# Kernel tuning notes

Measured on AMD Instinct MI355X. Metric: run time of the kernel, lower is better.

The kernel has to match this reference:

```python
import jax, jax.numpy as jnp
import numpy as np

D_K = 128
D_V = 128
SEQ_LEN = 2048


def setup_inputs() -> dict:
    key = jax.random.key(0)
    kq, kk, kv = jax.random.split(key, 3)
    q = jax.random.normal(kq, (SEQ_LEN, D_K), dtype=jnp.float32)
    k = jax.random.normal(kk, (SEQ_LEN, D_K), dtype=jnp.float32)
    v = jax.random.normal(kv, (SEQ_LEN, D_V), dtype=jnp.float32)
    return {"q": q, "k": k, "v": v}


def _step(carry, qkv):
    J, Svv, Sqv, Sqq, l = carry
    q, k, v = qkv
    l = l + 1
    fl = l.astype(J.dtype)
    # update_correlations: running means of outer products
    Svv = (fl - 1.0) / fl * Svv + jnp.outer(v, v) / fl
    Sqv = (fl - 1.0) / fl * Sqv + jnp.outer(q, v) / fl
    Sqq = (fl - 1.0) / fl * Sqq + jnp.outer(q, q) / fl

    first = l == 1

    # ecological params (J: [d_v, d_k], Sqv: [d_k, d_v], Sqq: [d_k, d_k])
    s_J = jnp.einsum('vk,kv->', J, Sqv)            # trace(J @ Sigma_qv)
    s_l = k @ Sqv @ v
    A_JJ = jnp.einsum('vk,kj,vj->', J, Sqq, J)     # trace(J Sqq J^T)
    A_ll = (v @ v) * (k @ Sqq @ k)
    A_Jl = v @ J @ Sqq @ k

    # safe denominators (unused branches must not produce NaN under where)
    A_JJ_s = jnp.where(first | (A_JJ == 0), 1.0, A_JJ)
    A_ll_s = jnp.where(first | (A_ll == 0), 1.0, A_ll)
    denom = A_JJ * A_ll - A_Jl ** 2
    denom_s = jnp.where(first | (denom == 0), 1.0, denom)

    margin = s_l - A_Jl * (s_J / A_JJ_s)

    wf = (A_ll * s_J - A_Jl * s_l) / denom_s
    wi = (A_JJ * s_l - A_Jl * s_J) / denom_s
    # nonnegativity constraints (check omega_i first, as in the source)
    wf_c = jnp.where(wi <= 0, s_J / A_JJ_s, jnp.where(wf <= 0, 0.0, wf))
    wi_c = jnp.where(wi <= 0, 0.0, jnp.where(wf <= 0, s_l / A_ll_s, wi))

    do_update = margin > 0
    vk = jnp.outer(v, k)
    J_upd = jnp.where(do_update, wf_c * J + wi_c * vk, J)
    J_new = jnp.where(first, vk, J_upd)
    updated = first | do_update

    # compute_cost with updated J and correlations
    cost = (0.5 * jnp.trace(Svv)
            - jnp.einsum('vk,kv->', J_new, Sqv)
            + 0.5 * jnp.einsum('vk,kj,vj->', J_new, Sqq, J_new))

    return (J_new, Svv, Sqv, Sqq, l), (cost, updated)


def _run(q, k, v):
    d_k, d_v = q.shape[-1], v.shape[-1]
    init = (jnp.zeros((d_v, d_k), q.dtype),
            jnp.zeros((d_v, d_v), q.dtype),
            jnp.zeros((d_k, d_v), q.dtype),
            jnp.zeros((d_k, d_k), q.dtype),
            jnp.int32(0))
    (J, _, _, _, _), (costs, updated) = jax.lax.scan(_step, init, (q, k, v))
    return costs, updated, J


def reference(q, k, v):
    return _run(q, k, v)
```

## Files before the change

### kernel.cpp

```cpp
#include <hip/hip_runtime.h>

#define SEQ 2048
#define D 128

typedef float v2f __attribute__((ext_vector_type(2)));
typedef float v4f __attribute__((ext_vector_type(4)));
#define LO2(v) __builtin_shufflevector(v, v, 0, 1)
#define HI2(v) __builtin_shufflevector(v, v, 2, 3)

__global__ __launch_bounds__(256) void precompute_kernel(
    const float* __restrict__ q, const float* __restrict__ k, const float* __restrict__ v,
    float* __restrict__ U, float* __restrict__ sl, float* __restrict__ kqq,
    float* __restrict__ vv, float* __restrict__ kq_adj, float* __restrict__ vv_adj,
    float* __restrict__ kU_adj, double* __restrict__ invl)
{
    const int s = blockIdx.x;
    const int tid = threadIdx.x;

    __shared__ float ks[D];
    __shared__ float vs[D];
    __shared__ float alpha[SEQ];
    __shared__ float red[8];
    __shared__ float upart[256];

    if (tid < D) ks[tid] = k[s * D + tid];
    else if (tid < 2 * D) vs[tid - D] = v[s * D + (tid - D)];
    __syncthreads();

    float p_a2 = 0.f, p_ab = 0.f;
    for (int i = tid; i <= s; i += 256) {
        const float4* qr = (const float4*)(q + (size_t)i * D);
        const float4* vr = (const float4*)(v + (size_t)i * D);
        float a = 0.f, b = 0.f;
#pragma unroll
        for (int j = 0; j < D / 4; ++j) {
            float4 q4 = qr[j];
            float4 v4 = vr[j];
            a += q4.x * ks[4 * j + 0] + q4.y * ks[4 * j + 1] + q4.z * ks[4 * j + 2] + q4.w * ks[4 * j + 3];
            b += v4.x * vs[4 * j + 0] + v4.y * vs[4 * j + 1] + v4.z * vs[4 * j + 2] + v4.w * vs[4 * j + 3];
        }
        alpha[i] = a;
        p_a2 += a * a;
        p_ab += a * b;
        if (i == s) vv[s] = b;
    }
#pragma unroll
    for (int off = 1; off < 64; off <<= 1) {
        p_a2 += __shfl_xor(p_a2, off);
        p_ab += __shfl_xor(p_ab, off);
    }
    const int wid = tid >> 6;
    if ((tid & 63) == 0) { red[wid] = p_a2; red[4 + wid] = p_ab; }
    __syncthreads();
    if (tid == 0) {
        kqq[s] = red[0] + red[1] + red[2] + red[3];
        sl[s]  = red[4] + red[5] + red[6] + red[7];
        invl[s] = 1.0 / (double)(s + 1);
    }

    if (tid < 64) {
        if (s + 1 < SEQ) {
            float p2 = ks[tid] * q[(size_t)(s + 1) * D + tid]
                     + ks[tid + 64] * q[(size_t)(s + 1) * D + 64 + tid];
#pragma unroll
            for (int off = 1; off < 64; off <<= 1) p2 += __shfl_xor(p2, off);
            if (tid == 0) kq_adj[s + 1] = p2;
        }
        if (s == 0 && tid == 0) { kq_adj[0] = 0.f; kU_adj[0] = 0.f; vv_adj[0] = 0.f; }
    } else if (tid < 128 && s > 0) {
        const int t2 = tid - 64;
        float p2 = vs[t2] * v[(size_t)(s - 1) * D + t2]
                 + vs[t2 + 64] * v[(size_t)(s - 1) * D + 64 + t2];
#pragma unroll
        for (int off = 1; off < 64; off <<= 1) p2 += __shfl_xor(p2, off);
        if (t2 == 0) vv_adj[s] = p2;
    }

    const int c = tid & (D - 1);
    const int h = tid >> 7;
    float a0 = 0.f, a1 = 0.f, a2 = 0.f, a3 = 0.f;
    int i = h;
    for (; i + 6 <= s; i += 8) {
        a0 = fmaf(q[(size_t)(i    ) * D + c], alpha[i    ], a0);
        a1 = fmaf(q[(size_t)(i + 2) * D + c], alpha[i + 2], a1);
        a2 = fmaf(q[(size_t)(i + 4) * D + c], alpha[i + 4], a2);
        a3 = fmaf(q[(size_t)(i + 6) * D + c], alpha[i + 6], a3);
    }
    for (; i <= s; i += 2) a0 = fmaf(q[(size_t)i * D + c], alpha[i], a0);
    upart[tid] = (a0 + a1) + (a2 + a3);
    __syncthreads();

    float kup = 0.f;
    if (tid < D) {
        const float uv = upart[tid] + upart[tid + D];
        U[(size_t)s * D + tid] = uv;
        if (s > 0) kup = uv * k[(size_t)(s - 1) * D + tid];
    }
#pragma unroll
    for (int off = 1; off < 64; off <<= 1) kup += __shfl_xor(kup, off);
    if (tid == 0)  red[0] = kup;
    if (tid == 64) red[1] = kup;
    __syncthreads();
    if (s > 0 && tid == 0) kU_adj[s] = red[0] + red[1];
}

#define DPP_ADD(x, ctrl) \
    ((x) + __int_as_float(__builtin_amdgcn_update_dpp(0, __float_as_int(x), (ctrl), 0xf, 0xf, true)))
#define REDUCE16(x) do { x = DPP_ADD(x, 0xB1); x = DPP_ADD(x, 0x4E); \
                         x = DPP_ADD(x, 0x141); x = DPP_ADD(x, 0x140); } while (0)

#define UPDATE_J(MODE, WF, WI)                                                \
    if ((MODE) == 2) {                                                        \
        const v2f wA = {vc4.x, vc4.x}, wB = {vc4.y, vc4.y};                   \
        const v2f wC = {vc4.z, vc4.z}, wD = {vc4.w, vc4.w};                   \
        jA0 = wA * k0_; jA1 = wA * k1_; jA2 = wA * k2_; jA3 = wA * k3_;       \
        jB0 = wB * k0_; jB1 = wB * k1_; jB2 = wB * k2_; jB3 = wB * k3_;       \
        jC0 = wC * k0_; jC1 = wC * k1_; jC2 = wC * k2_; jC3 = wC * k3_;       \
        jD0 = wD * k0_; jD1 = wD * k1_; jD2 = wD * k2_; jD3 = wD * k3_;       \
    } else if ((MODE) == 1) {                                                 \
        const v2f wf2 = {(WF), (WF)};                                         \
        const float sA = (WI) * vc4.x, sB = (WI) * vc4.y;                     \
        const float sC = (WI) * vc4.z, sD = (WI) * vc4.w;                     \
        const v2f wA = {sA, sA}, wB = {sB, sB}, wC = {sC, sC}, wD = {sD, sD}; \
        jA0 = __builtin_elementwise_fma(jA0, wf2, wA * k0_);                  \
        jA1 = __builtin_elementwise_fma(jA1, wf2, wA * k1_);                  \
        jA2 = __builtin_elementwise_fma(jA2, wf2, wA * k2_);                  \
        jA3 = __builtin_elementwise_fma(jA3, wf2, wA * k3_);                  \
        jB0 = __builtin_elementwise_fma(jB0, wf2, wB * k0_);                  \
        jB1 = __builtin_elementwise_fma(jB1, wf2, wB * k1_);                  \
        jB2 = __builtin_elementwise_fma(jB2, wf2, wB * k2_);                  \
        jB3 = __builtin_elementwise_fma(jB3, wf2, wB * k3_);                  \
        jC0 = __builtin_elementwise_fma(jC0, wf2, wC * k0_);                  \
        jC1 = __builtin_elementwise_fma(jC1, wf2, wC * k1_);                  \
        jC2 = __builtin_elementwise_fma(jC2, wf2, wC * k2_);                  \
        jC3 = __builtin_elementwise_fma(jC3, wf2, wC * k3_);                  \
        jD0 = __builtin_elementwise_fma(jD0, wf2, wD * k0_);                  \
        jD1 = __builtin_elementwise_fma(jD1, wf2, wD * k1_);                  \
        jD2 = __builtin_elementwise_fma(jD2, wf2, wD * k2_);                  \
        jD3 = __builtin_elementwise_fma(jD3, wf2, wD * k3_);                  \
    }

__global__ __launch_bounds__(1024, 4) void scan_kernel(
    const float* __restrict__ q, const float* __restrict__ k, const float* __restrict__ v,
    const float* __restrict__ U, const float* __restrict__ sl_arr,
    const float* __restrict__ kqq_arr, const float* __restrict__ vv_arr,
    const float* __restrict__ kq_adj, const float* __restrict__ vv_adj,
    const float* __restrict__ kU_adj, const double* __restrict__ invl_arr,
    float* __restrict__ out)
{
    const int tid  = threadIdx.x;
    const int lane = tid & 63;
    const int w    = __builtin_amdgcn_readfirstlane(tid >> 6);

    __shared__ float ring[3][4][160];
    __shared__ __align__(16) float wred[3][32][4];
    __shared__ __align__(16) float decLDS[3][4];

    const bool isj     = (tid >= 512);
    const int  jw      = w - 8;
    const int  i16     = lane & 15;
    const int  r4      = lane >> 4;
    const int  o       = 20 * (i16 >> 1) + 8 * (i16 & 1);
    const int  rb      = (jw << 4) + (r4 << 2);
    const int  vo      = 20 * jw + (r4 << 2);

    const bool stager  = (tid >= 128) && (tid < 512);
    const int  which   = (tid >> 7) - 1;
    const int  sidx    = tid & 127;
    const int  widx    = ((sidx >> 4) * 20) + (sidx & 15);

    const bool vstager = (tid >= 64) && (tid < 128);
    const int  s2      = tid & 63;
    const int  vc0     = 2 * s2;
    const int  vwidx   = 20 * (vc0 >> 4) + (vc0 & 15);

    v2f jA0 = {0.f, 0.f}, jA1 = jA0, jA2 = jA0, jA3 = jA0;
    v2f jB0 = jA0, jB1 = jA0, jB2 = jA0, jB3 = jA0;
    v2f jC0 = jA0, jC1 = jA0, jC2 = jA0, jC3 = jA0;
    v2f jD0 = jA0, jD1 = jA0, jD2 = jA0, jD3 = jA0;
    v4f vc4 = {0.f, 0.f, 0.f, 0.f}, vn4 = vc4;

    float gstage = 0.f;
    v2f   gv = {0.f, 0.f};
    if (stager) {
        if (which == 0) {
            ring[0][0][widx] = q[(size_t)1 * D + sidx];
            ring[1][0][widx] = q[(size_t)2 * D + sidx];
            gstage = q[(size_t)3 * D + sidx];
        } else if (which == 1) {
            ring[0][1][widx] = U[(size_t)1 * D + sidx];
            ring[1][1][widx] = U[(size_t)2 * D + sidx];
            gstage = U[(size_t)3 * D + sidx];
        } else {
            ring[0][2][widx] = k[sidx];
            ring[1][2][widx] = k[(size_t)1 * D + sidx];
            gstage = k[(size_t)2 * D + sidx];
        }
    } else if (vstager) {
        *(v2f*)&ring[0][3][vwidx] = *(const v2f*)&v[(size_t)1 * D + vc0];
        *(v2f*)&ring[1][3][vwidx] = *(const v2f*)&v[(size_t)2 * D + vc0];
        gv = *(const v2f*)&v[(size_t)3 * D + vc0];
    } else if (isj) {
        vc4 = *(const v4f*)&v[rb];
    }

    float dwf = 0.f, dwi = 1.f;
    int dmode = 2;
    if (tid == 0) { decLDS[0][0] = 0.f; decLDS[0][1] = 1.f; decLDS[0][2] = 2.f; decLDS[0][3] = 0.f; }

    double SJ = 0.0, AJJ = 0.0, trSvv = 0.0;
    if (w == 0) {
        const double sl0 = (double)sl_arr[0];
        const double kq0 = (double)kqq_arr[0];
        const double vv0 = (double)vv_arr[0];
        trSvv = vv0;
        SJ  = sl0;
        AJJ = vv0 * kq0;
        if (lane == 0) {
            out[0] = (float)((0.5 * trSvv - SJ + 0.5 * AJJ) * invl_arr[0]);
            out[SEQ] = 1.f;
        }
    }
    __syncthreads();

#define STEP_BODY(I, P, PN, PW)                                               \
{                                                                             \
    float c_sl = 0.f, c_kq = 0.f, c_vv = 0.f, c_kqa = 0.f, c_vva = 0.f,       \
          c_vvp = 0.f, c_kua = 0.f;                                           \
    double c_inv = 0.0;                                                       \
    if (w == 0) {                                                             \
        c_sl  = sl_arr[(I) + 1];  c_kq  = kqq_arr[(I) + 1];                   \
        c_vv  = vv_arr[(I) + 1];  c_kqa = kq_adj[(I) + 1];                    \
        c_vva = vv_adj[(I) + 1];  c_vvp = vv_arr[(I)];                        \
        c_kua = kU_adj[(I) + 1];  c_inv = invl_arr[(I) + 1];                  \
    }                                                                         \
    if (isj) {                                                                \
        const v4f Qa = ((const v4f*)&ring[P][0][o])[0];                       \
        const v4f Qb = ((const v4f*)&ring[P][0][o])[1];                       \
        const v4f Ua = ((const v4f*)&ring[P][1][o])[0];                       \
        const v4f Ub = ((const v4f*)&ring[P][1][o])[1];                       \
        vn4 = *((const v4f*)&ring[P][3][vo]);                                 \
        const v2f q0 = LO2(Qa), q1 = HI2(Qa), q2 = LO2(Qb), q3 = HI2(Qb);     \
        v2f aA = jA0 * q0, aB = jB0 * q0, aC = jC0 * q0, aD = jD0 * q0;       \
        aA = __builtin_elementwise_fma(jA1, q1, aA);                          \
        aB = __builtin_elementwise_fma(jB1, q1, aB);                          \
        aC = __builtin_elementwise_fma(jC1, q1, aC);                          \
        aD = __builtin_elementwise_fma(jD1, q1, aD);                          \
        aA = __builtin_elementwise_fma(jA2, q2, aA);                          \
        aB = __builtin_elementwise_fma(jB2, q2, aB);                          \
        aC = __builtin_elementwise_fma(jC2, q2, aC);                          \
        aD = __builtin_elementwise_fma(jD2, q2, aD);                          \
        aA = __builtin_elementwise_fma(jA3, q3, aA);                          \
        aB = __builtin_elementwise_fma(jB3, q3, aB);                          \
        aC = __builtin_elementwise_fma(jC3, q3, aC);                          \
        aD = __builtin_elementwise_fma(jD3, q3, aD);                          \
        float YqA = aA.x + aA.y, YqB = aB.x + aB.y;                           \
        float YqC = aC.x + aC.y, YqD = aD.x + aD.y;                           \
        const v2f u0 = LO2(Ua), u1 = HI2(Ua), u2 = LO2(Ub), u3 = HI2(Ub);     \
        v2f bA = jA0 * u0, bB = jB0 * u0, bC = jC0 * u0, bD = jD0 * u0;       \
        bA = __builtin_elementwise_fma(jA1, u1, bA);                          \
        bB = __builtin_elementwise_fma(jB1, u1, bB);                          \
        bC = __builtin_elementwise_fma(jC1, u1, bC);                          \
        bD = __builtin_elementwise_fma(jD1, u1, bD);                          \
        bA = __builtin_elementwise_fma(jA2, u2, bA);                          \
        bB = __builtin_elementwise_fma(jB2, u2, bB);                          \
        bC = __builtin_elementwise_fma(jC2, u2, bC);                          \
        bD = __builtin_elementwise_fma(jD2, u2, bD);                          \
        bA = __builtin_elementwise_fma(jA3, u3, bA);                          \
        bB = __builtin_elementwise_fma(jB3, u3, bB);                          \
        bC = __builtin_elementwise_fma(jC3, u3, bC);                          \
        bD = __builtin_elementwise_fma(jD3, u3, bD);                          \
        float YwA = bA.x + bA.y, YwB = bB.x + bB.y;                           \
        float YwC = bC.x + bC.y, YwD = bD.x + bD.y;                           \
        REDUCE16(YqA); REDUCE16(YqB); REDUCE16(YqC); REDUCE16(YqD);           \
        REDUCE16(YwA); REDUCE16(YwB); REDUCE16(YwC); REDUCE16(YwD);           \
        const float z1 = (vn4.x * YqA + vn4.y * YqB) + (vn4.z * YqC + vn4.w * YqD); \
        const float z2 = (YqA * YqA + YqB * YqB) + (YqC * YqC + YqD * YqD);   \
        const float z3 = (vc4.x * YqA + vc4.y * YqB) + (vc4.z * YqC + vc4.w * YqD); \
        const float z4 = (vn4.x * YwA + vn4.y * YwB) + (vn4.z * YwC + vn4.w * YwD); \
        if ((lane & 15) == 15)                                                \
            *(float4*)&wred[P][(jw << 2) | r4][0] = make_float4(z1, z2, z3, z4); \
    }                                                                         \
    __syncthreads();                                                          \
    if (stager) {                                                             \
        ring[PW][which][widx] = gstage;                                       \
        const int tq_ = ((I) + 4 < SEQ) ? (I) + 4 : SEQ - 1;                  \
        const int tk_ = ((I) + 3 < SEQ) ? (I) + 3 : SEQ - 1;                  \
        gstage = (which == 0) ? q[(size_t)tq_ * D + sidx]                     \
               : (which == 1) ? U[(size_t)tq_ * D + sidx]                     \
                              : k[(size_t)tk_ * D + sidx];                    \
    } else if (vstager) {                                                     \
        *(v2f*)&ring[PW][3][vwidx] = gv;                                      \
        const int tv_ = ((I) + 4 < SEQ) ? (I) + 4 : SEQ - 1;                  \
        gv = *(const v2f*)&v[(size_t)tv_ * D + vc0];                          \
    } else if (isj) {                                                         \
        const float4 df = *(const float4*)&decLDS[P][0];                      \
        const v4f Ka = ((const v4f*)&ring[P][2][o])[0];                       \
        const v4f Kb = ((const v4f*)&ring[P][2][o])[1];                       \
        const v2f k0_ = LO2(Ka), k1_ = HI2(Ka), k2_ = LO2(Kb), k3_ = HI2(Kb); \
        const float uwf = df.x, uwi = df.y;                                   \
        const int   umode = (int)df.z;                                        \
        UPDATE_J(umode, uwf, uwi)                                             \
        vc4 = vn4;                                                            \
    } else if (w == 0) {                                                      \
        const float4 wa = *(const float4*)&wred[P][lane & 15][0];             \
        const float4 wb = *(const float4*)&wred[P][16 + (lane & 15)][0];      \
        float4 ww = make_float4(wa.x + wb.x, wa.y + wb.y,                     \
                                wa.z + wb.z, wa.w + wb.w);                    \
        const float odwf = dwf, odwi = dwi;                                   \
        const int   odmode = dmode;                                           \
        REDUCE16(ww.x);                                                       \
        REDUCE16(ww.y);                                                       \
        REDUCE16(ww.z);                                                       \
        REDUCE16(ww.w);                                                       \
        double a_, b_;                                                        \
        if (odmode == 2)      { a_ = 0.0; b_ = 1.0; }                         \
        else if (odmode == 1) { a_ = (double)odwf; b_ = (double)odwi; }       \
        else                  { a_ = 1.0; b_ = 0.0; }                         \
        const double kqa = (double)c_kqa, vva = (double)c_vva;                \
        const double vvp = (double)c_vvp, kua = (double)c_kua;                \
        const double r1 = (double)ww.x, r2 = (double)ww.y;                    \
        const double r3 = (double)ww.z, r4_ = (double)ww.w;                   \
        const double Jqv  = a_ * r1 + b_ * (kqa * vva);                       \
        const double Jq2  = a_ * a_ * r2 + 2.0 * a_ * b_ * kqa * r3          \
                          + b_ * b_ * kqa * kqa * vvp;                        \
        const double AJl_ = a_ * r4_ + b_ * kua * vva;                        \
        trSvv += (double)c_vv;                                                \
        SJ    += Jqv;                                                         \
        AJJ   += Jq2;                                                         \
        const double s_l  = (double)c_sl;                                     \
        const double A_ll = (double)c_vv * (double)c_kq;                      \
        const double AJJ_s  = (AJJ == 0.0)  ? 1.0 : AJJ;                      \
        const double A_ll_s = (A_ll == 0.0) ? 1.0 : A_ll;                     \
        const double denom   = AJJ * A_ll - AJl_ * AJl_;                      \
        const double denom_s = (denom == 0.0) ? 1.0 : denom;                  \
        const double rden = 1.0 / denom_s;                                    \
        const double wf = (A_ll * SJ - AJl_ * s_l) * rden;                    \
        const double wi = (AJJ * s_l - AJl_ * SJ) * rden;                     \
        double wf_c, wi_c;                                                    \
        if (wi <= 0.0)      { wf_c = SJ / AJJ_s;  wi_c = 0.0; }               \
        else if (wf <= 0.0) { wf_c = 0.0;         wi_c = s_l / A_ll_s; }      \
        else                { wf_c = wf;          wi_c = wi; }                \
        const bool do_update = (s_l * AJJ_s - AJl_ * SJ) > 0.0;               \
        int mode;                                                             \
        if (do_update) {                                                      \
            mode = 1;                                                         \
            const double nSJ = wf_c * SJ + wi_c * s_l;                        \
            AJJ = wf_c * wf_c * AJJ + 2.0 * wf_c * wi_c * AJl_                \
                + wi_c * wi_c * A_ll;                                         \
            SJ = nSJ;                                                         \
        } else {                                                              \
            mode = 0;                                                         \
        }                                                                     \
        dwf = (float)wf_c; dwi = (float)wi_c; dmode = mode;                   \
        if (lane == 0) {                                                      \
            out[(I) + 1] = (float)((0.5 * trSvv - SJ + 0.5 * AJJ) * c_inv);   \
            out[SEQ + (I) + 1] = mode ? 1.f : 0.f;                            \
            *(float4*)&decLDS[PN][0] = make_float4(dwf, dwi, (float)mode, 0.f);\
        }                                                                     \
    }                                                                         \
}

    for (int i = 0; i + 2 < SEQ - 1; i += 3) {
        STEP_BODY(i,     0, 1, 2)
        STEP_BODY(i + 1, 1, 2, 0)
        STEP_BODY(i + 2, 2, 0, 1)
    }
    STEP_BODY(SEQ - 2, 0, 1, 2)
#undef STEP_BODY

    __syncthreads();
    if (isj) {
        const float4 df = *(const float4*)&decLDS[1][0];
        const float fwf = df.x, fwi = df.y;
        const int   fmode = (int)df.z;
        const v4f Ka = ((const v4f*)&ring[1][2][o])[0];
        const v4f Kb = ((const v4f*)&ring[1][2][o])[1];
        const v2f k0_ = LO2(Ka), k1_ = HI2(Ka), k2_ = LO2(Kb), k3_ = HI2(Kb);
        UPDATE_J(fmode, fwf, fwi)
        float* jb = out + 2 * SEQ + (size_t)rb * D + 8 * i16;
        *(v4f*)(jb + 0)         = __builtin_shufflevector(jA0, jA1, 0, 1, 2, 3);
        *(v4f*)(jb + 4)         = __builtin_shufflevector(jA2, jA3, 0, 1, 2, 3);
        *(v4f*)(jb + D + 0)     = __builtin_shufflevector(jB0, jB1, 0, 1, 2, 3);
        *(v4f*)(jb + D + 4)     = __builtin_shufflevector(jB2, jB3, 0, 1, 2, 3);
        *(v4f*)(jb + 2 * D + 0) = __builtin_shufflevector(jC0, jC1, 0, 1, 2, 3);
        *(v4f*)(jb + 2 * D + 4) = __builtin_shufflevector(jC2, jC3, 0, 1, 2, 3);
        *(v4f*)(jb + 3 * D + 0) = __builtin_shufflevector(jD0, jD1, 0, 1, 2, 3);
        *(v4f*)(jb + 3 * D + 4) = __builtin_shufflevector(jD2, jD3, 0, 1, 2, 3);
    }
}

extern "C" void kernel_launch(void* const* d_in, const int* in_sizes, int n_in,
                              void* d_out, int out_size, void* d_ws, size_t ws_size,
                              hipStream_t stream) {
    (void)in_sizes; (void)n_in; (void)out_size; (void)ws_size;
    const float* q = (const float*)d_in[0];
    const float* k = (const float*)d_in[1];
    const float* v = (const float*)d_in[2];
    float* out = (float*)d_out;

    float* U      = (float*)d_ws;
    float* sl     = U + (size_t)SEQ * D;
    float* kqq    = sl + SEQ;
    float* vv     = kqq + SEQ;
    float* kq_adj = vv + SEQ;
    float* vv_adj = kq_adj + SEQ;
    float* kU_adj = vv_adj + SEQ;
    double* invl  = (double*)(kU_adj + SEQ);

    precompute_kernel<<<SEQ, 256, 0, stream>>>(q, k, v, U, sl, kqq, vv,
                                               kq_adj, vv_adj, kU_adj, invl);
    scan_kernel<<<1, 1024, 0, stream>>>(q, k, v, U, sl, kqq, vv,
                                        kq_adj, vv_adj, kU_adj, invl, out);
}
```

Baseline: 2.533 ms.

## Deepen prefetch pipeline, prefetch scalars into registers, use lighter barriers

Each global stager now keeps three steps of q/U/k/v in flight in registers instead of one. The per-step scalar arrays are prefetched by wave 0 into register rings during the J phase, so they are no longer loaded on the decision critical path. The K fragment load moves before the barrier. __syncthreads is replaced by an LDS-only waitcnt plus s_barrier, and the two divisions are computed without branches. This cuts global-load latency and barrier cost in the serial 2048-step loop, at the price of more registers and a barrier that does not wait for outstanding global memory operations.

```diff
diff --git a/kernel.cpp b/kernel.cpp
--- a/kernel.cpp
+++ b/kernel.cpp
@@ -108,6 +108,9 @@
     ((x) + __int_as_float(__builtin_amdgcn_update_dpp(0, __float_as_int(x), (ctrl), 0xf, 0xf, true)))
 #define REDUCE16(x) do { x = DPP_ADD(x, 0xB1); x = DPP_ADD(x, 0x4E); \
                          x = DPP_ADD(x, 0x141); x = DPP_ADD(x, 0x140); } while (0)
+
+#define BARRIER() do { asm volatile("s_waitcnt lgkmcnt(0)" ::: "memory"); \
+                       __builtin_amdgcn_s_barrier(); } while (0)
 
 #define UPDATE_J(MODE, WF, WI)                                                \
     if ((MODE) == 2) {                                                        \
@@ -180,26 +183,39 @@
     v2f jD0 = jA0, jD1 = jA0, jD2 = jA0, jD3 = jA0;
     v4f vc4 = {0.f, 0.f, 0.f, 0.f}, vn4 = vc4;
 
-    float gstage = 0.f;
-    v2f   gv = {0.f, 0.f};
+    float gs[3] = {0.f, 0.f, 0.f};
+    v2f   gv[3] = {{0.f,0.f},{0.f,0.f},{0.f,0.f}};
+    float p_sl[3] = {0,0,0}, p_kq[3] = {0,0,0}, p_vv[3] = {0,0,0};
+    float p_kqa[3] = {0,0,0}, p_vva[3] = {0,0,0}, p_vvp[3] = {0,0,0};
+    float p_kua[3] = {0,0,0};
+    double p_inv[3] = {0,0,0};
+
     if (stager) {
         if (which == 0) {
             ring[0][0][widx] = q[(size_t)1 * D + sidx];
             ring[1][0][widx] = q[(size_t)2 * D + sidx];
-            gstage = q[(size_t)3 * D + sidx];
+            gs[2] = q[(size_t)3 * D + sidx];
+            gs[0] = q[(size_t)4 * D + sidx];
+            gs[1] = q[(size_t)5 * D + sidx];
         } else if (which == 1) {
             ring[0][1][widx] = U[(size_t)1 * D + sidx];
             ring[1][1][widx] = U[(size_t)2 * D + sidx];
-            gstage = U[(size_t)3 * D + sidx];
+            gs[2] = U[(size_t)3 * D + sidx];
+            gs[0] = U[(size_t)4 * D + sidx];
+            gs[1] = U[(size_t)5 * D + sidx];
         } else {
             ring[0][2][widx] = k[sidx];
             ring[1][2][widx] = k[(size_t)1 * D + sidx];
-            gstage = k[(size_t)2 * D + sidx];
+            gs[2] = k[(size_t)2 * D + sidx];
+            gs[0] = k[(size_t)3 * D + sidx];
+            gs[1] = k[(size_t)4 * D + sidx];
         }
     } else if (vstager) {
         *(v2f*)&ring[0][3][vwidx] = *(const v2f*)&v[(size_t)1 * D + vc0];
         *(v2f*)&ring[1][3][vwidx] = *(const v2f*)&v[(size_t)2 * D + vc0];
-        gv = *(const v2f*)&v[(size_t)3 * D + vc0];
+        gv[2] = *(const v2f*)&v[(size_t)3 * D + vc0];
+        gv[0] = *(const v2f*)&v[(size_t)4 * D + vc0];
+        gv[1] = *(const v2f*)&v[(size_t)5 * D + vc0];
     } else if (isj) {
         vc4 = *(const v4f*)&v[rb];
     }
@@ -210,6 +226,13 @@
 
     double SJ = 0.0, AJJ = 0.0, trSvv = 0.0;
     if (w == 0) {
+        p_sl[0]  = sl_arr[1];  p_kq[0]  = kqq_arr[1]; p_vv[0] = vv_arr[1];
+        p_kqa[0] = kq_adj[1];  p_vva[0] = vv_adj[1];  p_kua[0] = kU_adj[1];
+        p_inv[0] = invl_arr[1]; p_vvp[0] = vv_arr[0];
+        p_sl[1]  = sl_arr[2];  p_kq[1]  = kqq_arr[2]; p_vv[1] = vv_arr[2];
+        p_kqa[1] = kq_adj[2];  p_vva[1] = vv_adj[2];  p_kua[1] = kU_adj[2];
+        p_inv[1] = invl_arr[2]; p_vvp[1] = vv_arr[1];
+
         const double sl0 = (double)sl_arr[0];
         const double kq0 = (double)kqq_arr[0];
         const double vv0 = (double)vv_arr[0];
@@ -221,25 +244,20 @@
             out[SEQ] = 1.f;
         }
     }
-    __syncthreads();
+    BARRIER();
 
 #define STEP_BODY(I, P, PN, PW)                                               \
 {                                                                             \
-    float c_sl = 0.f, c_kq = 0.f, c_vv = 0.f, c_kqa = 0.f, c_vva = 0.f,       \
-          c_vvp = 0.f, c_kua = 0.f;                                           \
-    double c_inv = 0.0;                                                       \
-    if (w == 0) {                                                             \
-        c_sl  = sl_arr[(I) + 1];  c_kq  = kqq_arr[(I) + 1];                   \
-        c_vv  = vv_arr[(I) + 1];  c_kqa = kq_adj[(I) + 1];                    \
-        c_vva = vv_adj[(I) + 1];  c_vvp = vv_arr[(I)];                        \
-        c_kua = kU_adj[(I) + 1];  c_inv = invl_arr[(I) + 1];                  \
-    }                                                                         \
+    v2f k0_ = {0.f, 0.f}, k1_ = k0_, k2_ = k0_, k3_ = k0_;                    \
     if (isj) {                                                                \
         const v4f Qa = ((const v4f*)&ring[P][0][o])[0];                       \
         const v4f Qb = ((const v4f*)&ring[P][0][o])[1];                       \
         const v4f Ua = ((const v4f*)&ring[P][1][o])[0];                       \
         const v4f Ub = ((const v4f*)&ring[P][1][o])[1];                       \
+        const v4f Ka = ((const v4f*)&ring[P][2][o])[0];                       \
+        const v4f Kb = ((const v4f*)&ring[P][2][o])[1];                       \
         vn4 = *((const v4f*)&ring[P][3][vo]);                                 \
+        k0_ = LO2(Ka); k1_ = HI2(Ka); k2_ = LO2(Kb); k3_ = HI2(Kb);           \
         const v2f q0 = LO2(Qa), q1 = HI2(Qa), q2 = LO2(Qb), q3 = HI2(Qb);     \
         v2f aA = jA0 * q0, aB = jB0 * q0, aC = jC0 * q0, aD = jD0 * q0;       \
         aA = __builtin_elementwise_fma(jA1, q1, aA);                          \
@@ -280,29 +298,36 @@
         const float z4 = (vn4.x * YwA + vn4.y * YwB) + (vn4.z * YwC + vn4.w * YwD); \
         if ((lane & 15) == 15)                                                \
             *(float4*)&wred[P][(jw << 2) | r4][0] = make_float4(z1, z2, z3, z4); \
+    } else if (w == 0) {                                                      \
+        const int t_ = ((I) + 3 < SEQ) ? (I) + 3 : SEQ - 1;                   \
+        p_sl[PW]  = sl_arr[t_];   p_kq[PW]  = kqq_arr[t_];                    \
+        p_vv[PW]  = vv_arr[t_];   p_kqa[PW] = kq_adj[t_];                     \
+        p_vva[PW] = vv_adj[t_];   p_kua[PW] = kU_adj[t_];                     \
+        p_inv[PW] = invl_arr[t_]; p_vvp[PW] = p_vv[PN];                       \
     }                                                                         \
-    __syncthreads();                                                          \
+    BARRIER();                                                                \
     if (stager) {                                                             \
-        ring[PW][which][widx] = gstage;                                       \
-        const int tq_ = ((I) + 4 < SEQ) ? (I) + 4 : SEQ - 1;                  \
-        const int tk_ = ((I) + 3 < SEQ) ? (I) + 3 : SEQ - 1;                  \
-        gstage = (which == 0) ? q[(size_t)tq_ * D + sidx]                     \
+        ring[PW][which][widx] = gs[PW];                                       \
+        const int tq_ = ((I) + 6 < SEQ) ? (I) + 6 : SEQ - 1;                  \
+        const int tk_ = ((I) + 5 < SEQ) ? (I) + 5 : SEQ - 1;                  \
+        gs[PW] = (which == 0) ? q[(size_t)tq_ * D + sidx]                     \
                : (which == 1) ? U[(size_t)tq_ * D + sidx]                     \
                               : k[(size_t)tk_ * D + sidx];                    \
     } else if (vstager) {                                                     \
-        *(v2f*)&ring[PW][3][vwidx] = gv;                                      \
-        const int tv_ = ((I) + 4 < SEQ) ? (I) + 4 : SEQ - 1;                  \
-        gv = *(const v2f*)&v[(size_t)tv_ * D + vc0];                          \
+        *(v2f*)&ring[PW][3][vwidx] = gv[PW];                                  \
+        const int tv_ = ((I) + 6 < SEQ) ? (I) + 6 : SEQ - 1;                  \
+        gv[PW] = *(const v2f*)&v[(size_t)tv_ * D + vc0];                      \
     } else if (isj) {                                                         \
         const float4 df = *(const float4*)&decLDS[P][0];                      \
-        const v4f Ka = ((const v4f*)&ring[P][2][o])[0];                       \
-        const v4f Kb = ((const v4f*)&ring[P][2][o])[1];                       \
-        const v2f k0_ = LO2(Ka), k1_ = HI2(Ka), k2_ = LO2(Kb), k3_ = HI2(Kb); \
         const float uwf = df.x, uwi = df.y;                                   \
         const int   umode = (int)df.z;                                        \
         UPDATE_J(umode, uwf, uwi)                                             \
         vc4 = vn4;                                                            \
     } else if (w == 0) {                                                      \
+        const float c_sl  = p_sl[P],  c_kq  = p_kq[P],  c_vv  = p_vv[P];      \
+        const float c_kqa = p_kqa[P], c_vva = p_vva[P], c_vvp = p_vvp[P];     \
+        const float c_kua = p_kua[P];                                         \
+        const double c_inv = p_inv[P];                                        \
         const float4 wa = *(const float4*)&wred[P][lane & 15][0];             \
         const float4 wb = *(const float4*)&wred[P][16 + (lane & 15)][0];      \
         float4 ww = make_float4(wa.x + wb.x, wa.y + wb.y,                     \
@@ -332,15 +357,17 @@
         const double A_ll = (double)c_vv * (double)c_kq;                      \
         const double AJJ_s  = (AJJ == 0.0)  ? 1.0 : AJJ;                      \
         const double A_ll_s = (A_ll == 0.0) ? 1.0 : A_ll;                     \
+        const double divJ = SJ / AJJ_s;     \
+        const double divL = s_l / A_ll_s;   \
         const double denom   = AJJ * A_ll - AJl_ * AJl_;                      \
         const double denom_s = (denom == 0.0) ? 1.0 : denom;                  \
         const double rden = 1.0 / denom_s;                                    \
         const double wf = (A_ll * SJ - AJl_ * s_l) * rden;                    \
         const double wi = (AJJ * s_l - AJl_ * SJ) * rden;                     \
         double wf_c, wi_c;                                                    \
-        if (wi <= 0.0)      { wf_c = SJ / AJJ_s;  wi_c = 0.0; }               \
-        else if (wf <= 0.0) { wf_c = 0.0;         wi_c = s_l / A_ll_s; }      \
-        else                { wf_c = wf;          wi_c = wi; }                \
+        if (wi <= 0.0)      { wf_c = divJ; wi_c = 0.0; }                      \
+        else if (wf <= 0.0) { wf_c = 0.0;  wi_c = divL; }                     \
+        else                { wf_c = wf;   wi_c = wi; }                       \
         const bool do_update = (s_l * AJJ_s - AJl_ * SJ) > 0.0;               \
         int mode;                                                             \
         if (do_update) {                                                      \
@@ -369,7 +396,7 @@
     STEP_BODY(SEQ - 2, 0, 1, 2)
 #undef STEP_BODY
 
-    __syncthreads();
+    BARRIER();
     if (isj) {
         const float4 df = *(const float4*)&decLDS[1][0];
         const float fwf = df.x, fwi = df.y;
```

After: 2.615 ms. 1.03x slower.
